# Kernel tuning notes

Hardware: AMD Instinct MI355X
Metric: run time of the kernel (lower is better)

## Reference

```python
import jax, jax.numpy as jnp
import numpy as np

EMB = 512
H = 8
DK = EMB // H          # 64
MAX_SEQ = 768
TOPK = MAX_SEQ // 2    # 384


def setup_inputs() -> dict:
    key = jax.random.key(0)
    ks = jax.random.split(key, 16)
    B, S, E = 1, MAX_SEQ, EMB

    def w(k, shape):
        return jax.random.normal(k, shape, dtype=jnp.float32) * 0.02

    return {
        "x": jax.random.normal(ks[0], (B, S, E), dtype=jnp.float32),
        # main attention projections (Linear weights stored as (in, out))
        "Wq": w(ks[1], (E, E)), "bq": w(ks[2], (E,)),
        "Wk": w(ks[3], (E, E)), "bk": w(ks[4], (E,)),
        "Wv": w(ks[5], (E, E)), "bv": w(ks[6], (E,)),
        "Wo": w(ks[7], (E, E)), "bo": w(ks[8], (E,)),
        # indexer projections: wq -> (E, H*DK)=(E,E), wk -> (E, DK), weights_proj -> (E, H)
        "iq_W": w(ks[9], (E, H * DK)), "iq_b": w(ks[10], (H * DK,)),
        "ik_W": w(ks[11], (E, DK)),    "ik_b": w(ks[12], (DK,)),
        "wp_W": w(ks[13], (E, H)),     "wp_b": w(ks[14], (H,)),
    }


def reference(x, Wq, bq, Wk, bk, Wv, bv, Wo, bo, iq_W, iq_b, ik_W, ik_b, wp_W, wp_b):
    B, S, E = x.shape
    scaling = 1.0 / np.sqrt(DK)

    def split_heads(z):  # (B,S,E) -> (B,H,S,DK)
        return z.reshape(B, S, H, DK).transpose(0, 2, 1, 3)

    Q = split_heads(x @ Wq + bq)
    K = split_heads(x @ Wk + bk)
    V = split_heads(x @ Wv + bv)

    # --- indexer: per-token relevance scores ---
    q_idx = (x @ iq_W + iq_b).reshape(B, S, H, DK).transpose(0, 2, 1, 3)  # (B,H,S,DK)
    k_idx = x @ ik_W + ik_b                                               # (B,S,DK)
    w_idx = x @ wp_W + wp_b                                               # (B,S,H)
    score = jax.nn.relu(jnp.einsum('bhsd,btd->bhst', q_idx, k_idx))       # (B,H,S,S)
    indexer_score = jnp.einsum('bhst,bsh->bst', score, w_idx)             # (B,S,S)

    # --- top-k selection (set-equivalent to argpartition in the original) ---
    topk_idx = jax.lax.top_k(indexer_score, TOPK)[1]                      # (B,S,TOPK) int32

    # --- gather sparse K/V per query token ---
    def gather_b(Zb, idxb):  # Zb:(H,S,DK), idxb:(S,TOPK) -> (H,S,TOPK,DK)
        return Zb[:, idxb, :]
    K_s = jax.vmap(gather_b)(K, topk_idx)  # (B,H,S,TOPK,DK)
    V_s = jax.vmap(gather_b)(V, topk_idx)  # (B,H,S,TOPK,DK)

    # --- sparse attention over selected tokens ---
    sc = jnp.einsum('bhsd,bhskd->bhsk', Q, K_s) * scaling  # (B,H,S,TOPK)
    wts = jax.nn.softmax(sc, axis=-1)
    attn = jnp.einsum('bhsk,bhskd->bhsd', wts, V_s)        # (B,H,S,DK)

    out = attn.transpose(0, 2, 1, 3).reshape(B, S, E) @ Wo + bo
    return out
```

## Files before the change

kernel.cpp:

```cpp
#include <hip/hip_runtime.h>
#include <hip/hip_bf16.h>
#include <math.h>

#define S 768
#define E 512
#define H 8
#define DK 64
#define TOPK 384

typedef short bf16x8 __attribute__((ext_vector_type(8)));
typedef float f32x4 __attribute__((ext_vector_type(4)));

__device__ __forceinline__ unsigned short f2bf(float x) {
  unsigned u = __float_as_uint(x);
  unsigned r = u + 0x7FFFu + ((u >> 16) & 1u);
  return (unsigned short)(r >> 16);
}
__device__ __forceinline__ float bf2f(unsigned short h) {
  return __uint_as_float(((unsigned)h) << 16);
}
__device__ __forceinline__ void split1(float x, unsigned short& h, unsigned short& l) {
  h = f2bf(x);
  l = f2bf(x - bf2f(h));
}

__device__ __forceinline__ void mfma3(f32x4& d, bf16x8 ah, bf16x8 al,
                                      bf16x8 bh, bf16x8 bl) {
  d = __builtin_amdgcn_mfma_f32_16x16x32_bf16(ah, bh, d, 0, 0, 0);
  d = __builtin_amdgcn_mfma_f32_16x16x32_bf16(ah, bl, d, 0, 0, 0);
  d = __builtin_amdgcn_mfma_f32_16x16x32_bf16(al, bh, d, 0, 0, 0);
}
__device__ __forceinline__ void mfma2(f32x4& d, bf16x8 ah, bf16x8 al, bf16x8 bh) {
  d = __builtin_amdgcn_mfma_f32_16x16x32_bf16(ah, bh, d, 0, 0, 0);
  d = __builtin_amdgcn_mfma_f32_16x16x32_bf16(al, bh, d, 0, 0, 0);
}

__device__ __forceinline__ bf16x8 ldfrag(const unsigned short* p) {
  return *reinterpret_cast<const bf16x8*>(p);
}

struct PrepTab {
  const float* src[8];
  unsigned short* hi[8];
  unsigned short* lo[8];
};

__global__ __launch_bounds__(256) void prep_kernel(PrepTab t) {
  const int seg = blockIdx.z;
  const int rows = (seg == 0) ? 768 : 512;
  const int cols = (seg == 5) ? 64 : ((seg == 6) ? 8 : 512);
  const int tx = (seg == 6) ? 2 : ((cols + 31) >> 5);
  const int ty = rows >> 5;
  if ((int)blockIdx.x >= tx || (int)blockIdx.y >= ty) return;
  const int r0 = blockIdx.y * 32, c0 = blockIdx.x * 32;
  const int tid = threadIdx.x;
  const int rl = tid >> 3, c4 = (tid & 7) << 2;
  const float* src = t.src[seg];
  if (seg == 0) {
    float4 v = *(const float4*)(src + (size_t)(r0 + rl) * cols + c0 + c4);
    unsigned short h[4], l[4];
    split1(v.x, h[0], l[0]); split1(v.y, h[1], l[1]);
    split1(v.z, h[2], l[2]); split1(v.w, h[3], l[3]);
    size_t off = (size_t)(r0 + rl) * cols + c0 + c4;
    *(ushort4*)(t.hi[seg] + off) = make_ushort4(h[0], h[1], h[2], h[3]);
    *(ushort4*)(t.lo[seg] + off) = make_ushort4(l[0], l[1], l[2], l[3]);
  } else {
    __shared__ float ts[32][33];
    #pragma unroll
    for (int j = 0; j < 4; ++j) {
      int c = c4 + j;
      ts[rl][c] = (c0 + c < cols) ? src[(size_t)(r0 + rl) * cols + c0 + c] : 0.0f;
    }
    __syncthreads();
    float v0 = ts[c4 + 0][rl], v1 = ts[c4 + 1][rl];
    float v2 = ts[c4 + 2][rl], v3 = ts[c4 + 3][rl];
    unsigned short h[4], l[4];
    split1(v0, h[0], l[0]); split1(v1, h[1], l[1]);
    split1(v2, h[2], l[2]); split1(v3, h[3], l[3]);
    size_t off = (size_t)(c0 + rl) * 512 + r0 + c4;
    *(ushort4*)(t.hi[seg] + off) = make_ushort4(h[0], h[1], h[2], h[3]);
    *(ushort4*)(t.lo[seg] + off) = make_ushort4(l[0], l[1], l[2], l[3]);
  }
}

struct ProjTab {
  const unsigned short* whi[6];
  const unsigned short* wlo[6];
  const float* bias[6];
};

__global__ __launch_bounds__(256) void proj_mfma_kernel(
    const unsigned short* __restrict__ Xhi, const unsigned short* __restrict__ Xlo,
    ProjTab pt,
    unsigned short* __restrict__ Qhi, unsigned short* __restrict__ Qlo,
    unsigned short* __restrict__ Khi, unsigned short* __restrict__ Klo,
    unsigned short* __restrict__ VThi,
    unsigned short* __restrict__ QIhi, unsigned short* __restrict__ QIlo,
    unsigned short* __restrict__ KIhi, unsigned short* __restrict__ KIlo,
    float* __restrict__ WI) {
  __shared__ __align__(16) unsigned short Ah[64][72];
  __shared__ __align__(16) unsigned short Al[64][72];
  __shared__ __align__(16) unsigned short Bh[64][72];
  __shared__ __align__(16) unsigned short Bl[64][72];
  const int bx = blockIdx.x;
  int seg, nt;
  if (bx < 32) { seg = bx >> 3; nt = bx & 7; }
  else         { seg = 4 + (bx - 32); nt = 0; }
  const int m0 = blockIdx.y * 64;
  const int n0 = nt * 64;
  const int tid = threadIdx.x;
  const int lane = tid & 63;
  const int wave = tid >> 6;
  const int mq = (wave >> 1) << 5;
  const int nq = (wave & 1) << 5;
  const int l15 = lane & 15;
  const int q8 = (lane >> 4) << 3;
  const int q4 = (lane >> 4) << 2;
  const unsigned short* Whi = pt.whi[seg];
  const unsigned short* Wlo = pt.wlo[seg];

  f32x4 acc[2][2] = {};
  for (int cc = 0; cc < 8; ++cc) {
    const int k0 = cc << 6;
    #pragma unroll
    for (int j = 0; j < 2; ++j) {
      const int flat = tid + (j << 8);
      const int mm = flat >> 3;
      const int kc = (flat & 7) << 3;
      const size_t ga = (size_t)(m0 + mm) * 512 + k0 + kc;
      const size_t gb = (size_t)(n0 + mm) * 512 + k0 + kc;
      *(bf16x8*)&Ah[mm][kc] = ldfrag(Xhi + ga);
      *(bf16x8*)&Al[mm][kc] = ldfrag(Xlo + ga);
      *(bf16x8*)&Bh[mm][kc] = ldfrag(Whi + gb);
      *(bf16x8*)&Bl[mm][kc] = ldfrag(Wlo + gb);
    }
    __syncthreads();
    #pragma unroll
    for (int ki = 0; ki < 64; ki += 32) {
      const int kk = ki + q8;
      bf16x8 ah0 = *(const bf16x8*)&Ah[mq + l15][kk];
      bf16x8 al0 = *(const bf16x8*)&Al[mq + l15][kk];
      bf16x8 ah1 = *(const bf16x8*)&Ah[mq + 16 + l15][kk];
      bf16x8 al1 = *(const bf16x8*)&Al[mq + 16 + l15][kk];
      bf16x8 bh0 = *(const bf16x8*)&Bh[nq + l15][kk];
      bf16x8 bl0 = *(const bf16x8*)&Bl[nq + l15][kk];
      bf16x8 bh1 = *(const bf16x8*)&Bh[nq + 16 + l15][kk];
      bf16x8 bl1 = *(const bf16x8*)&Bl[nq + 16 + l15][kk];
      mfma3(acc[0][0], ah0, al0, bh0, bl0);
      mfma3(acc[0][1], ah0, al0, bh1, bl1);
      mfma3(acc[1][0], ah1, al1, bh0, bl0);
      mfma3(acc[1][1], ah1, al1, bh1, bl1);
    }
    __syncthreads();
  }

  const float* bias = pt.bias[seg];
  #pragma unroll
  for (int ntt = 0; ntt < 2; ++ntt) {
    const int nloc = n0 + nq + ntt * 16 + l15;
    const float bv = (seg == 5 && nloc >= 8) ? 0.0f : bias[nloc];
    #pragma unroll
    for (int mt = 0; mt < 2; ++mt) {
      #pragma unroll
      for (int r = 0; r < 4; ++r) {
        const int m = m0 + mq + mt * 16 + q4 + r;
        const float v = acc[mt][ntt][r] + bv;
        unsigned short h16, l16;
        if (seg == 0) {
          split1(v, h16, l16);
          Qhi[(size_t)m * 512 + nloc] = h16;
          Qlo[(size_t)m * 512 + nloc] = l16;
        } else if (seg == 1) {
          const int hh = nloc >> 6, dd = nloc & 63;
          split1(v, h16, l16);
          Khi[((size_t)hh * S + m) * 64 + dd] = h16;
          Klo[((size_t)hh * S + m) * 64 + dd] = l16;
        } else if (seg == 2) {
          VThi[((size_t)(nloc >> 6) * 64 + (nloc & 63)) * S + m] = f2bf(v);
        } else if (seg == 3) {
          split1(v, h16, l16);
          QIhi[(size_t)m * 512 + nloc] = h16;
          QIlo[(size_t)m * 512 + nloc] = l16;
        } else if (seg == 4) {
          split1(v, h16, l16);
          KIhi[(size_t)m * 64 + nloc] = h16;
          KIlo[(size_t)m * 64 + nloc] = l16;
        } else {
          if (nloc < 8) WI[(size_t)m * 8 + nloc] = v;
        }
      }
    }
  }
}

__global__ __launch_bounds__(256) void indexer_mfma_kernel(
    const unsigned short* __restrict__ QIhi, const unsigned short* __restrict__ QIlo,
    const unsigned short* __restrict__ KIhi, const unsigned short* __restrict__ KIlo,
    const float* __restrict__ WI, float* __restrict__ ISC) {
  __shared__ __align__(16) unsigned short Qh[32][136];
  __shared__ __align__(16) unsigned short Ql[32][136];
  __shared__ float wis[32][8];
  const int s0 = blockIdx.y * 32, t0 = blockIdx.x * 64;
  const int tid = threadIdx.x;
  const int lane = tid & 63;
  const int wave = tid >> 6;
  const int mq = (wave >> 1) << 4;
  const int nqb = (wave & 1) << 5;
  const int l15 = lane & 15;
  const int q8 = (lane >> 4) << 3;
  const int q4 = (lane >> 4) << 2;
  wis[tid >> 3][tid & 7] = WI[(size_t)(s0 + (tid >> 3)) * 8 + (tid & 7)];

  const size_t brow0 = (size_t)(t0 + nqb + l15) * 64;
  const size_t brow1 = (size_t)(t0 + nqb + 16 + l15) * 64;
  bf16x8 kfh[2][2], kfl[2][2];
  #pragma unroll
  for (int kk = 0; kk < 2; ++kk) {
    const int kb = kk * 32 + q8;
    kfh[kk][0] = ldfrag(KIhi + brow0 + kb);
    kfl[kk][0] = ldfrag(KIlo + brow0 + kb);
    kfh[kk][1] = ldfrag(KIhi + brow1 + kb);
    kfl[kk][1] = ldfrag(KIlo + brow1 + kb);
  }

  const int smm = tid >> 3;
  const int skc = (tid & 7) << 4;
  float accI[2][4] = {};
  for (int hp = 0; hp < 4; ++hp) {
    __syncthreads();
    {
      const size_t g = (size_t)(s0 + smm) * 512 + hp * 128 + skc;
      *(bf16x8*)&Qh[smm][skc]     = ldfrag(QIhi + g);
      *(bf16x8*)&Qh[smm][skc + 8] = ldfrag(QIhi + g + 8);
      *(bf16x8*)&Ql[smm][skc]     = ldfrag(QIlo + g);
      *(bf16x8*)&Ql[smm][skc + 8] = ldfrag(QIlo + g + 8);
    }
    __syncthreads();
    #pragma unroll
    for (int hh = 0; hh < 2; ++hh) {
      const int h = hp * 2 + hh;
      f32x4 d[2] = {};
      #pragma unroll
      for (int kk = 0; kk < 2; ++kk) {
        const int ka = hh * 64 + kk * 32 + q8;
        bf16x8 ah = *(const bf16x8*)&Qh[mq + l15][ka];
        bf16x8 al = *(const bf16x8*)&Ql[mq + l15][ka];
        mfma3(d[0], ah, al, kfh[kk][0], kfl[kk][0]);
        mfma3(d[1], ah, al, kfh[kk][1], kfl[kk][1]);
      }
      #pragma unroll
      for (int r = 0; r < 4; ++r) {
        const float w = wis[mq + q4 + r][h];
        accI[0][r] = fmaf(fmaxf(d[0][r], 0.0f), w, accI[0][r]);
        accI[1][r] = fmaf(fmaxf(d[1][r], 0.0f), w, accI[1][r]);
      }
    }
  }
  #pragma unroll
  for (int ntt = 0; ntt < 2; ++ntt)
    #pragma unroll
    for (int r = 0; r < 4; ++r)
      ISC[(size_t)(s0 + mq + q4 + r) * S + t0 + nqb + ntt * 16 + l15] = accI[ntt][r];
}

__global__ __launch_bounds__(256) void topk_kernel(
    const float* __restrict__ ISC, unsigned* __restrict__ Mask,
    float* __restrict__ Sum, float* __restrict__ ATTacc) {
  __shared__ unsigned ordv[768];
  __shared__ int hist[256];
  __shared__ int gsum[16];
  __shared__ int sc[256];
  __shared__ unsigned mw[24];
  __shared__ unsigned sh_prefix;
  __shared__ int sh_R;
  const int s = blockIdx.x;
  const int tid = threadIdx.x;
  for (int i = tid; i < 768; i += 256) {
    float f = ISC[s * 768 + i] + 0.0f;
    unsigned u = __float_as_uint(f);
    ordv[i] = (u & 0x80000000u) ? ~u : (u | 0x80000000u);
  }
  {
    const float4 z4 = {0.0f, 0.0f, 0.0f, 0.0f};
    if (tid < 128) *(float4*)(ATTacc + (size_t)s * 512 + tid * 4) = z4;
  }
  if (tid < 24) mw[tid] = 0u;
  if (tid < H) Sum[tid * S + s] = 0.0f;
  if (tid == 0) { sh_prefix = 0u; sh_R = TOPK; }
  __syncthreads();
  for (int pass = 0; pass < 4; ++pass) {
    const int shift = 24 - pass * 8;
    hist[tid] = 0;
    __syncthreads();
    const unsigned pm = (pass == 0) ? 0u : (0xFFFFFFFFu << (shift + 8));
    const unsigned pref = sh_prefix;
    for (int i = tid; i < 768; i += 256) {
      unsigned o = ordv[i];
      if ((o & pm) == pref) atomicAdd(&hist[(o >> shift) & 255], 1);
    }
    __syncthreads();
    if (tid < 16) {
      int t = 0;
      #pragma unroll
      for (int k = 0; k < 16; ++k) t += hist[tid * 16 + k];
      gsum[tid] = t;
    }
    __syncthreads();
    if (tid == 0) {
      int R = sh_R;
      int G = 0;
      int g = 15;
      for (; g > 0; --g) {
        if (G + gsum[g] >= R) break;
        G += gsum[g];
      }
      int b = 15;
      for (; b > 0; --b) {
        int c = hist[g * 16 + b];
        if (G + c >= R) break;
        G += c;
      }
      sh_prefix = sh_prefix | ((unsigned)(g * 16 + b) << shift);
      sh_R = R - G;
    }
    __syncthreads();
  }
  const unsigned thr = sh_prefix;
  const int need_eq = sh_R;
  const int base = tid * 3;
  unsigned o0 = ordv[base], o1 = ordv[base + 1], o2 = ordv[base + 2];
  int c = (o0 == thr) + (o1 == thr) + (o2 == thr);
  sc[tid] = c;
  __syncthreads();
  for (int off = 1; off < 256; off <<= 1) {
    int v = (tid >= off) ? sc[tid - off] : 0;
    __syncthreads();
    sc[tid] += v;
    __syncthreads();
  }
  int rank = sc[tid] - c;
  if (o0 > thr || (o0 == thr && rank < need_eq))
    atomicOr(&mw[base >> 5], 1u << (base & 31));
  if (o0 == thr) ++rank;
  if (o1 > thr || (o1 == thr && rank < need_eq))
    atomicOr(&mw[(base + 1) >> 5], 1u << ((base + 1) & 31));
  if (o1 == thr) ++rank;
  if (o2 > thr || (o2 == thr && rank < need_eq))
    atomicOr(&mw[(base + 2) >> 5], 1u << ((base + 2) & 31));
  __syncthreads();
  if (tid < 24) Mask[s * 24 + tid] = mw[tid];
}

__global__ __launch_bounds__(512) void sattn_kernel(
    const unsigned short* __restrict__ Qhi, const unsigned short* __restrict__ Qlo,
    const unsigned short* __restrict__ Khi, const unsigned short* __restrict__ Klo,
    const unsigned short* __restrict__ VThi,
    const unsigned* __restrict__ Mask, float* __restrict__ ATTacc,
    float* __restrict__ Sum) {
  __shared__ __align__(16) unsigned short Ksh[64][72];
  __shared__ __align__(16) unsigned short Ksl[64][72];
  __shared__ __align__(16) unsigned short Vsh[64][72];
  __shared__ __align__(16) unsigned short Pshi[64][72];
  __shared__ __align__(16) unsigned short Pslo[64][72];
  __shared__ unsigned msk[64][6];
  __shared__ float rsumf[64];
  const int ks = blockIdx.x;
  const int s0 = blockIdx.y * 64;
  const int h  = blockIdx.z;
  const int tid = threadIdx.x;
  const int lane = tid & 63;
  const int wave = tid >> 6;
  const int l15 = lane & 15;
  const int q8 = (lane >> 4) << 3;
  const int q4 = (lane >> 4) << 2;
  const int mq = (wave >> 1) << 4;
  const int nqq = (wave & 1) << 4;
  const int db = (wave & 1) << 5;

  if (tid < 384) msk[tid & 63][tid >> 6] =
      Mask[(size_t)(s0 + (tid & 63)) * 24 + ks * 6 + (tid >> 6)];
  if (tid < 64) rsumf[tid] = 0.0f;

  const size_t qrow = (size_t)(s0 + mq + l15) * 512 + h * 64;
  bf16x8 qh0 = ldfrag(Qhi + qrow + 0 + q8);
  bf16x8 ql0 = ldfrag(Qlo + qrow + 0 + q8);
  bf16x8 qh1 = ldfrag(Qhi + qrow + 32 + q8);
  bf16x8 ql1 = ldfrag(Qlo + qrow + 32 + q8);

  f32x4 oacc[2] = {};
  for (int ct = 0; ct < 3; ++ct) {
    const int tch = ks * 192 + ct * 64;
    __syncthreads();
    {
      const int tr = tid >> 3;
      const int kc = (tid & 7) << 3;
      const size_t gk = ((size_t)h * S + tch + tr) * 64 + kc;
      *(bf16x8*)&Ksh[tr][kc] = ldfrag(Khi + gk);
      *(bf16x8*)&Ksl[tr][kc] = ldfrag(Klo + gk);
      *(bf16x8*)&Vsh[tr][kc] =
          ldfrag(VThi + ((size_t)h * 64 + tr) * S + tch + kc);
    }
    __syncthreads();
    float esum[4] = {0.0f, 0.0f, 0.0f, 0.0f};
    #pragma unroll
    for (int cp = 0; cp < 2; ++cp) {
      const int tcol = nqq + cp * 32;
      f32x4 d = {0.0f, 0.0f, 0.0f, 0.0f};
      bf16x8 bh0 = *(const bf16x8*)&Ksh[tcol + l15][q8];
      bf16x8 bl0 = *(const bf16x8*)&Ksl[tcol + l15][q8];
      bf16x8 bh1 = *(const bf16x8*)&Ksh[tcol + l15][32 + q8];
      bf16x8 bl1 = *(const bf16x8*)&Ksl[tcol + l15][32 + q8];
      mfma3(d, qh0, ql0, bh0, bl0);
      mfma3(d, qh1, ql1, bh1, bl1);
      const int tl = ct * 64 + tcol + l15;
      #pragma unroll
      for (int r = 0; r < 4; ++r) {
        const int srow = mq + q4 + r;
        const unsigned w = msk[srow][tl >> 5];
        float e = ((w >> (tl & 31)) & 1u) ? __expf(d[r] * 0.125f) : 0.0f;
        unsigned short h16, l16;
        split1(e, h16, l16);
        Pshi[srow][tcol + l15] = h16;
        Pslo[srow][tcol + l15] = l16;
        esum[r] += e;
      }
    }
    float v0 = esum[0], v1 = esum[1], v2 = esum[2], v3 = esum[3];
    #pragma unroll
    for (int off = 1; off < 16; off <<= 1) {
      v0 += __shfl_xor(v0, off);
      v1 += __shfl_xor(v1, off);
      v2 += __shfl_xor(v2, off);
      v3 += __shfl_xor(v3, off);
    }
    if (l15 == 0) {
      atomicAdd(&rsumf[mq + q4 + 0], v0);
      atomicAdd(&rsumf[mq + q4 + 1], v1);
      atomicAdd(&rsumf[mq + q4 + 2], v2);
      atomicAdd(&rsumf[mq + q4 + 3], v3);
    }
    __syncthreads();
    #pragma unroll
    for (int kk = 0; kk < 64; kk += 32) {
      bf16x8 pah = *(const bf16x8*)&Pshi[mq + l15][kk + q8];
      bf16x8 pal = *(const bf16x8*)&Pslo[mq + l15][kk + q8];
      #pragma unroll
      for (int dt = 0; dt < 2; ++dt) {
        bf16x8 vbh = *(const bf16x8*)&Vsh[db + dt * 16 + l15][kk + q8];
        mfma2(oacc[dt], pah, pal, vbh);
      }
    }
  }
  #pragma unroll
  for (int dt = 0; dt < 2; ++dt) {
    const int dd = db + dt * 16 + l15;
    #pragma unroll
    for (int r = 0; r < 4; ++r) {
      const int s = s0 + mq + q4 + r;
      atomicAdd(&ATTacc[(size_t)s * E + h * DK + dd], oacc[dt][r]);
    }
  }
  __syncthreads();
  if (tid < 64) atomicAdd(&Sum[(size_t)h * S + s0 + tid], rsumf[tid]);
}

__global__ __launch_bounds__(512) void out_mfma_kernel(
    const float* __restrict__ ATTacc, const float* __restrict__ Sum,
    const unsigned short* __restrict__ WoThi,
    const float* __restrict__ bo, float* __restrict__ out) {
  __shared__ float AccL[16][65];
  __shared__ float ivs[16][8];
  const int tid512 = threadIdx.x;
  const int wave8 = tid512 >> 6;
  const int z = wave8 >> 2;
  const int wave = wave8 & 3;
  const int lane = tid512 & 63;
  const int m0 = blockIdx.y * 16;
  const int n0 = blockIdx.x * 64 + wave * 16;
  const int l15 = lane & 15;
  const int q8 = (lane >> 4) << 3;
  const int q4 = (lane >> 4) << 2;
  if (tid512 < 128) {
    const int r = tid512 >> 3, hh = tid512 & 7;
    ivs[r][hh] = 1.0f / Sum[(size_t)hh * S + m0 + r];
  }
  __syncthreads();
  const size_t arow = (size_t)(m0 + l15) * 512;
  const size_t brow = (size_t)(n0 + l15) * 512;
  int ko = (z << 8) + q8;
  bf16x8 cah, cal;
  {
    const float inv0 = ivs[l15][(ko >> 6) & 7];
    float4 a = *(const float4*)(ATTacc + arow + ko);
    float4 b = *(const float4*)(ATTacc + arow + ko + 4);
    float v[8] = {a.x, a.y, a.z, a.w, b.x, b.y, b.z, b.w};
    #pragma unroll
    for (int i = 0; i < 8; ++i) {
      unsigned short hh, ll;
      split1(v[i] * inv0, hh, ll);
      cah[i] = (short)hh; cal[i] = (short)ll;
    }
  }
  bf16x8 cbh = ldfrag(WoThi + brow + ko);
  f32x4 acc = {};
  #pragma unroll
  for (int it = 0; it < 8; ++it) {
    const int kn = ko + 32;
    float4 na = *(const float4*)(ATTacc + arow + kn);
    float4 nb = *(const float4*)(ATTacc + arow + kn + 4);
    bf16x8 nbh = ldfrag(WoThi + brow + kn);
    mfma2(acc, cah, cal, cbh);
    const float invn = ivs[l15][(kn >> 6) & 7];
    float v[8] = {na.x, na.y, na.z, na.w, nb.x, nb.y, nb.z, nb.w};
    #pragma unroll
    for (int i = 0; i < 8; ++i) {
      unsigned short hh, ll;
      split1(v[i] * invn, hh, ll);
      cah[i] = (short)hh; cal[i] = (short)ll;
    }
    cbh = nbh;
    ko = kn;
  }
  if (z == 1) {
    #pragma unroll
    for (int r = 0; r < 4; ++r)
      AccL[q4 + r][wave * 16 + l15] = acc[r];
  }
  __syncthreads();
  if (z == 0) {
    const int n = n0 + l15;
    const float bv = bo[n];
    #pragma unroll
    for (int r = 0; r < 4; ++r)
      out[(size_t)(m0 + q4 + r) * 512 + n] =
          acc[r] + AccL[q4 + r][wave * 16 + l15] + bv;
  }
}

extern "C" void kernel_launch(void* const* d_in, const int* in_sizes, int n_in,
                              void* d_out, int out_size, void* d_ws, size_t ws_size,
                              hipStream_t stream) {
  const float* x    = (const float*)d_in[0];
  const float* Wq   = (const float*)d_in[1];
  const float* bq   = (const float*)d_in[2];
  const float* Wk   = (const float*)d_in[3];
  const float* bk   = (const float*)d_in[4];
  const float* Wv   = (const float*)d_in[5];
  const float* bv   = (const float*)d_in[6];
  const float* Wo   = (const float*)d_in[7];
  const float* bo   = (const float*)d_in[8];
  const float* iqW  = (const float*)d_in[9];
  const float* iqb  = (const float*)d_in[10];
  const float* ikW  = (const float*)d_in[11];
  const float* ikb  = (const float*)d_in[12];
  const float* wpW  = (const float*)d_in[13];
  const float* wpb  = (const float*)d_in[14];

  float* ws = (float*)d_ws;
  float* WI   = ws;
  float* ISC  = WI + S * H;
  unsigned* Mask = (unsigned*)(ISC + S * S);
  float* Sum  = (float*)(Mask + S * 24);
  float* ATTacc = Sum + H * S;
  unsigned short* u = (unsigned short*)(ATTacc + S * E);
  unsigned short* Xhi  = u;             u += S * E;
  unsigned short* Xlo  = u;             u += S * E;
  unsigned short* Qhi  = u;             u += S * E;
  unsigned short* Qlo  = u;             u += S * E;
  unsigned short* Khi  = u;             u += S * E;
  unsigned short* Klo  = u;             u += S * E;
  unsigned short* VThi = u;             u += S * E;
  unsigned short* QIhi = u;             u += S * E;
  unsigned short* QIlo = u;             u += S * E;
  unsigned short* KIhi = u;             u += S * DK;
  unsigned short* KIlo = u;             u += S * DK;
  unsigned short* WTq_hi = u;           u += E * E;
  unsigned short* WTk_hi = u;           u += E * E;
  unsigned short* WTv_hi = u;           u += E * E;
  unsigned short* WTiq_hi = u;          u += E * E;
  unsigned short* WTik_hi = u;          u += 64 * E;
  unsigned short* WTwp_hi = u;          u += 64 * E;
  unsigned short* WTo_hi = u;           u += E * E;
  unsigned short* WTq_lo = u;           u += E * E;
  unsigned short* WTk_lo = u;           u += E * E;
  unsigned short* WTv_lo = u;           u += E * E;
  unsigned short* WTiq_lo = u;          u += E * E;
  unsigned short* WTik_lo = u;          u += 64 * E;
  unsigned short* WTwp_lo = u;          u += 64 * E;
  unsigned short* WTo_lo = u;           u += E * E;

  PrepTab prep;
  prep.src[0] = x;    prep.hi[0] = Xhi;     prep.lo[0] = Xlo;
  prep.src[1] = Wq;   prep.hi[1] = WTq_hi;  prep.lo[1] = WTq_lo;
  prep.src[2] = Wk;   prep.hi[2] = WTk_hi;  prep.lo[2] = WTk_lo;
  prep.src[3] = Wv;   prep.hi[3] = WTv_hi;  prep.lo[3] = WTv_lo;
  prep.src[4] = iqW;  prep.hi[4] = WTiq_hi; prep.lo[4] = WTiq_lo;
  prep.src[5] = ikW;  prep.hi[5] = WTik_hi; prep.lo[5] = WTik_lo;
  prep.src[6] = wpW;  prep.hi[6] = WTwp_hi; prep.lo[6] = WTwp_lo;
  prep.src[7] = Wo;   prep.hi[7] = WTo_hi;  prep.lo[7] = WTo_lo;

  ProjTab pt;
  pt.whi[0] = WTq_hi;  pt.wlo[0] = WTq_lo;  pt.bias[0] = bq;
  pt.whi[1] = WTk_hi;  pt.wlo[1] = WTk_lo;  pt.bias[1] = bk;
  pt.whi[2] = WTv_hi;  pt.wlo[2] = WTv_lo;  pt.bias[2] = bv;
  pt.whi[3] = WTiq_hi; pt.wlo[3] = WTiq_lo; pt.bias[3] = iqb;
  pt.whi[4] = WTik_hi; pt.wlo[4] = WTik_lo; pt.bias[4] = ikb;
  pt.whi[5] = WTwp_hi; pt.wlo[5] = WTwp_lo; pt.bias[5] = wpb;

  prep_kernel<<<dim3(16, 24, 8), dim3(256), 0, stream>>>(prep);
  proj_mfma_kernel<<<dim3(34, S / 64), dim3(256), 0, stream>>>(
      Xhi, Xlo, pt, Qhi, Qlo, Khi, Klo, VThi, QIhi, QIlo, KIhi, KIlo, WI);
  indexer_mfma_kernel<<<dim3(S / 64, S / 32), dim3(256), 0, stream>>>(
      QIhi, QIlo, KIhi, KIlo, WI, ISC);
  topk_kernel<<<dim3(S), dim3(256), 0, stream>>>(ISC, Mask, Sum, ATTacc);
  sattn_kernel<<<dim3(4, S / 64, H), dim3(512), 0, stream>>>(
      Qhi, Qlo, Khi, Klo, VThi, Mask, ATTacc, Sum);
  out_mfma_kernel<<<dim3(8, 48), dim3(512), 0, stream>>>(
      ATTacc, Sum, WTo_hi, bo, (float*)d_out);
}
```

Baseline: 149.9 us.

## Register-prefetch next tiles in GEMM/indexer/attention loops and stage output A-tile in LDS

In the projection GEMM, indexer and sparse attention kernels, the next K-chunk's global loads are issued into registers before the current chunk is computed, so global latency overlaps with the MFMA work (software double buffering through registers). In the output projection kernel, the normalized attention rows are split into bf16 hi/lo once, cooperatively, into shared memory. The per-wave redundant reload and split of the A operand is dropped, since four waves previously each converted the same rows. This costs more registers and extra LDS, which may reduce occupancy.

```diff
diff --git a/kernel.cpp b/kernel.cpp
--- a/kernel.cpp
+++ b/kernel.cpp
@@ -119,20 +119,34 @@
   const unsigned short* Whi = pt.whi[seg];
   const unsigned short* Wlo = pt.wlo[seg];
 
+  const int mm0 = tid >> 3,          kc0 = (tid & 7) << 3;
+  const int mm1 = (tid + 256) >> 3,  kc1 = ((tid + 256) & 7) << 3;
+  const size_t ga0 = (size_t)(m0 + mm0) * 512 + kc0;
+  const size_t gb0 = (size_t)(n0 + mm0) * 512 + kc0;
+  const size_t ga1 = (size_t)(m0 + mm1) * 512 + kc1;
+  const size_t gb1 = (size_t)(n0 + mm1) * 512 + kc1;
+
+  bf16x8 rah0 = ldfrag(Xhi + ga0), ral0 = ldfrag(Xlo + ga0);
+  bf16x8 rbh0 = ldfrag(Whi + gb0), rbl0 = ldfrag(Wlo + gb0);
+  bf16x8 rah1 = ldfrag(Xhi + ga1), ral1 = ldfrag(Xlo + ga1);
+  bf16x8 rbh1 = ldfrag(Whi + gb1), rbl1 = ldfrag(Wlo + gb1);
+
   f32x4 acc[2][2] = {};
   for (int cc = 0; cc < 8; ++cc) {
-    const int k0 = cc << 6;
-    #pragma unroll
-    for (int j = 0; j < 2; ++j) {
-      const int flat = tid + (j << 8);
-      const int mm = flat >> 3;
-      const int kc = (flat & 7) << 3;
-      const size_t ga = (size_t)(m0 + mm) * 512 + k0 + kc;
-      const size_t gb = (size_t)(n0 + mm) * 512 + k0 + kc;
-      *(bf16x8*)&Ah[mm][kc] = ldfrag(Xhi + ga);
-      *(bf16x8*)&Al[mm][kc] = ldfrag(Xlo + ga);
-      *(bf16x8*)&Bh[mm][kc] = ldfrag(Whi + gb);
-      *(bf16x8*)&Bl[mm][kc] = ldfrag(Wlo + gb);
+    *(bf16x8*)&Ah[mm0][kc0] = rah0;
+    *(bf16x8*)&Al[mm0][kc0] = ral0;
+    *(bf16x8*)&Bh[mm0][kc0] = rbh0;
+    *(bf16x8*)&Bl[mm0][kc0] = rbl0;
+    *(bf16x8*)&Ah[mm1][kc1] = rah1;
+    *(bf16x8*)&Al[mm1][kc1] = ral1;
+    *(bf16x8*)&Bh[mm1][kc1] = rbh1;
+    *(bf16x8*)&Bl[mm1][kc1] = rbl1;
+    if (cc < 7) {
+      const size_t o = (size_t)(cc + 1) << 6;
+      rah0 = ldfrag(Xhi + ga0 + o); ral0 = ldfrag(Xlo + ga0 + o);
+      rbh0 = ldfrag(Whi + gb0 + o); rbl0 = ldfrag(Wlo + gb0 + o);
+      rah1 = ldfrag(Xhi + ga1 + o); ral1 = ldfrag(Xlo + ga1 + o);
+      rbh1 = ldfrag(Whi + gb1 + o); rbl1 = ldfrag(Wlo + gb1 + o);
     }
     __syncthreads();
     #pragma unroll
@@ -225,15 +239,25 @@
 
   const int smm = tid >> 3;
   const int skc = (tid & 7) << 4;
+  const size_t qbase = (size_t)(s0 + smm) * 512 + skc;
+  bf16x8 rq0 = ldfrag(QIhi + qbase);
+  bf16x8 rq1 = ldfrag(QIhi + qbase + 8);
+  bf16x8 rq2 = ldfrag(QIlo + qbase);
+  bf16x8 rq3 = ldfrag(QIlo + qbase + 8);
+
   float accI[2][4] = {};
   for (int hp = 0; hp < 4; ++hp) {
     __syncthreads();
-    {
-      const size_t g = (size_t)(s0 + smm) * 512 + hp * 128 + skc;
-      *(bf16x8*)&Qh[smm][skc]     = ldfrag(QIhi + g);
-      *(bf16x8*)&Qh[smm][skc + 8] = ldfrag(QIhi + g + 8);
-      *(bf16x8*)&Ql[smm][skc]     = ldfrag(QIlo + g);
-      *(bf16x8*)&Ql[smm][skc + 8] = ldfrag(QIlo + g + 8);
+    *(bf16x8*)&Qh[smm][skc]     = rq0;
+    *(bf16x8*)&Qh[smm][skc + 8] = rq1;
+    *(bf16x8*)&Ql[smm][skc]     = rq2;
+    *(bf16x8*)&Ql[smm][skc + 8] = rq3;
+    if (hp < 3) {
+      const size_t g = qbase + (size_t)(hp + 1) * 128;
+      rq0 = ldfrag(QIhi + g);
+      rq1 = ldfrag(QIhi + g + 8);
+      rq2 = ldfrag(QIlo + g);
+      rq3 = ldfrag(QIlo + g + 8);
     }
     __syncthreads();
     #pragma unroll
@@ -387,18 +411,24 @@
   bf16x8 qh1 = ldfrag(Qhi + qrow + 32 + q8);
   bf16x8 ql1 = ldfrag(Qlo + qrow + 32 + q8);
 
+  const int tr = tid >> 3;
+  const int kc = (tid & 7) << 3;
+  const size_t gkbase = ((size_t)h * S + ks * 192 + tr) * 64 + kc;
+  const size_t gvbase = ((size_t)h * 64 + tr) * S + ks * 192 + kc;
+  bf16x8 rkh = ldfrag(Khi + gkbase);
+  bf16x8 rkl = ldfrag(Klo + gkbase);
+  bf16x8 rv  = ldfrag(VThi + gvbase);
+
   f32x4 oacc[2] = {};
   for (int ct = 0; ct < 3; ++ct) {
-    const int tch = ks * 192 + ct * 64;
-    __syncthreads();
-    {
-      const int tr = tid >> 3;
-      const int kc = (tid & 7) << 3;
-      const size_t gk = ((size_t)h * S + tch + tr) * 64 + kc;
-      *(bf16x8*)&Ksh[tr][kc] = ldfrag(Khi + gk);
-      *(bf16x8*)&Ksl[tr][kc] = ldfrag(Klo + gk);
-      *(bf16x8*)&Vsh[tr][kc] =
-          ldfrag(VThi + ((size_t)h * 64 + tr) * S + tch + kc);
+    __syncthreads();
+    *(bf16x8*)&Ksh[tr][kc] = rkh;
+    *(bf16x8*)&Ksl[tr][kc] = rkl;
+    *(bf16x8*)&Vsh[tr][kc] = rv;
+    if (ct < 2) {
+      rkh = ldfrag(Khi + gkbase + (size_t)(ct + 1) * 4096);
+      rkl = ldfrag(Klo + gkbase + (size_t)(ct + 1) * 4096);
+      rv  = ldfrag(VThi + gvbase + (size_t)(ct + 1) * 64);
     }
     __syncthreads();
     float esum[4] = {0.0f, 0.0f, 0.0f, 0.0f};
@@ -470,6 +500,8 @@
     const float* __restrict__ bo, float* __restrict__ out) {
   __shared__ float AccL[16][65];
   __shared__ float ivs[16][8];
+  __shared__ __align__(16) unsigned short Ahi[16][520];
+  __shared__ __align__(16) unsigned short Alo[16][520];
   const int tid512 = threadIdx.x;
   const int wave8 = tid512 >> 6;
   const int z = wave8 >> 2;
@@ -485,41 +517,35 @@
     ivs[r][hh] = 1.0f / Sum[(size_t)hh * S + m0 + r];
   }
   __syncthreads();
-  const size_t arow = (size_t)(m0 + l15) * 512;
+  {
+    const int row = tid512 >> 5;
+    const int kb = (tid512 & 31) << 4;
+    const float inv = ivs[row][kb >> 6];
+    const float* src = ATTacc + (size_t)(m0 + row) * 512 + kb;
+    float4 a0 = *(const float4*)(src);
+    float4 a1 = *(const float4*)(src + 4);
+    float4 a2 = *(const float4*)(src + 8);
+    float4 a3 = *(const float4*)(src + 12);
+    float v[16] = {a0.x, a0.y, a0.z, a0.w, a1.x, a1.y, a1.z, a1.w,
+                   a2.x, a2.y, a2.z, a2.w, a3.x, a3.y, a3.z, a3.w};
+    #pragma unroll
+    for (int i = 0; i < 16; ++i) {
+      unsigned short hh, ll;
+      split1(v[i] * inv, hh, ll);
+      Ahi[row][kb + i] = hh;
+      Alo[row][kb + i] = ll;
+    }
+  }
+  __syncthreads();
   const size_t brow = (size_t)(n0 + l15) * 512;
-  int ko = (z << 8) + q8;
-  bf16x8 cah, cal;
-  {
-    const float inv0 = ivs[l15][(ko >> 6) & 7];
-    float4 a = *(const float4*)(ATTacc + arow + ko);
-    float4 b = *(const float4*)(ATTacc + arow + ko + 4);
-    float v[8] = {a.x, a.y, a.z, a.w, b.x, b.y, b.z, b.w};
-    #pragma unroll
-    for (int i = 0; i < 8; ++i) {
-      unsigned short hh, ll;
-      split1(v[i] * inv0, hh, ll);
-      cah[i] = (short)hh; cal[i] = (short)ll;
-    }
-  }
-  bf16x8 cbh = ldfrag(WoThi + brow + ko);
   f32x4 acc = {};
   #pragma unroll
   for (int it = 0; it < 8; ++it) {
-    const int kn = ko + 32;
-    float4 na = *(const float4*)(ATTacc + arow + kn);
-    float4 nb = *(const float4*)(ATTacc + arow + kn + 4);
-    bf16x8 nbh = ldfrag(WoThi + brow + kn);
-    mfma2(acc, cah, cal, cbh);
-    const float invn = ivs[l15][(kn >> 6) & 7];
-    float v[8] = {na.x, na.y, na.z, na.w, nb.x, nb.y, nb.z, nb.w};
-    #pragma unroll
-    for (int i = 0; i < 8; ++i) {
-      unsigned short hh, ll;
-      split1(v[i] * invn, hh, ll);
-      cah[i] = (short)hh; cal[i] = (short)ll;
-    }
-    cbh = nbh;
-    ko = kn;
+    const int ko = (z << 8) + (it << 5) + q8;
+    bf16x8 ah = *(const bf16x8*)&Ahi[l15][ko];
+    bf16x8 al = *(const bf16x8*)&Alo[l15][ko];
+    bf16x8 bh = ldfrag(WoThi + brow + ko);
+    mfma2(acc, ah, al, bh);
   }
   if (z == 1) {
     #pragma unroll
```

New measurement: 139.5 us. 6.9% less time.
